# Performance work log

Hardware: AMD Instinct MI355X
Metric: run time of the kernel (lower is better)

The kernel has to match this reference:

```python
import jax, jax.numpy as jnp
import numpy as np


def _gcn_conv(h_in, W, b, src, dst, dinv):
    # GCNConv with symmetric normalization and self-loops:
    # out_i = sum_{j->i} dinv_j*dinv_i * (x_j W) + dinv_i^2 * (x_i W) + b
    n = h_in.shape[0]
    h = h_in @ W  # [N, C_out] -- transform before aggregation (PyG order)
    coef = dinv[src] * dinv[dst]  # [E]
    agg = jax.ops.segment_sum(h[src] * coef[:, None], dst, num_segments=n)
    return agg + h * (dinv * dinv)[:, None] + b


def setup_inputs() -> dict:
    key = jax.random.key(0)
    ks = jax.random.split(key, 9)
    N, E = 100000, 1600000
    C_in, C_h, C_out = 256, 128, 64
    x = jax.random.normal(ks[0], (N, C_in), dtype=jnp.float32)
    edge_index = jax.random.randint(ks[1], (2, E), 0, N, dtype=jnp.int64)
    eps = jax.random.normal(ks[2], (N, C_out), dtype=jnp.float32)
    s = 1.0 / np.sqrt(C_in)
    W1 = jax.random.uniform(ks[3], (C_in, C_h), jnp.float32, -s, s)
    b1 = jnp.zeros((C_h,), jnp.float32)
    sh = 1.0 / np.sqrt(C_h)
    Wmu = jax.random.uniform(ks[4], (C_h, C_out), jnp.float32, -sh, sh)
    bmu = jnp.zeros((C_out,), jnp.float32)
    Wlv = jax.random.uniform(ks[5], (C_h, C_out), jnp.float32, -sh, sh)
    blv = jnp.zeros((C_out,), jnp.float32)
    return {"x": x, "edge_index": edge_index, "eps": eps,
            "W1": W1, "b1": b1, "Wmu": Wmu, "bmu": bmu,
            "Wlv": Wlv, "blv": blv}


def reference(x, edge_index, eps, W1, b1, Wmu, bmu, Wlv, blv):
    n = x.shape[0]
    src, dst = edge_index[0], edge_index[1]
    # degree with self-loops (each node gets +1)
    deg = jax.ops.segment_sum(jnp.ones_like(dst, dtype=x.dtype), dst,
                              num_segments=n) + 1.0
    dinv = jax.lax.rsqrt(deg)
    # encoder (eval mode: dropout is identity)
    h = jax.nn.relu(_gcn_conv(x, W1, b1, src, dst, dinv))
    mu = _gcn_conv(h, Wmu, bmu, src, dst, dinv)
    logvar = _gcn_conv(h, Wlv, blv, src, dst, dinv)
    # reparameterization with provided noise: z = mu + eps * exp(0.5*logvar)
    z = mu + eps * jnp.exp(0.5 * logvar)
    # inner-product decoder on the given edges: sigmoid(<z_i, z_j>)
    dec = jax.nn.sigmoid(jnp.sum(z[src] * z[dst], axis=1))
    return z, mu, logvar, dec
```

## Files before the change

### kernel.cpp

```cpp
#include <hip/hip_runtime.h>
#include <hip/hip_bf16.h>

#define MAXD 64
#define NPB 128
#define BSHIFT 7
#define EB 8192
#define NBMAX 1024

typedef __attribute__((ext_vector_type(8))) short bf16x8;
typedef __attribute__((ext_vector_type(4))) float f32x4;

__device__ __forceinline__ float blo(unsigned u){ return __uint_as_float(u << 16); }
__device__ __forceinline__ float bhi(unsigned u){ return __uint_as_float(u & 0xffff0000u); }
__device__ __forceinline__ short cvbf(float f){ return (short)__bfloat16_as_ushort(__float2bfloat16(f)); }
__device__ __forceinline__ unsigned pk2(float a, float b){
  unsigned la = (unsigned)__bfloat16_as_ushort(__float2bfloat16(a));
  unsigned lb = (unsigned)__bfloat16_as_ushort(__float2bfloat16(b));
  return la | (lb << 16);
}

__global__ __launch_bounds__(256) void k_tr_all(const float* __restrict__ W1,
                                                const float* __restrict__ Wmu,
                                                const float* __restrict__ Wlv,
                                                __hip_bfloat16* __restrict__ W1T,
                                                __hip_bfloat16* __restrict__ WcT){
  int i = blockIdx.x * 256 + threadIdx.x;
  if (i < 32768){
    int k = i >> 7, c = i & 127;
    W1T[(size_t)c * 256 + k] = __float2bfloat16(W1[i]);
  } else if (i < 40960){
    int j = i - 32768;
    int k = j >> 6, c = j & 63;
    WcT[(size_t)c * 128 + k] = __float2bfloat16(Wmu[j]);
  } else if (i < 49152){
    int j = i - 40960;
    int k = j >> 6, c = j & 63;
    WcT[(size_t)(64 + c) * 128 + k] = __float2bfloat16(Wlv[j]);
  }
}

#define LDP 40
template<bool AF32>
__device__ __forceinline__ void gemm_body(short* As, short* Bs, const void* __restrict__ Av,
                                          const __hip_bfloat16* __restrict__ BT,
                                          __hip_bfloat16* __restrict__ C,
                                          int M, int K, int bid){
  int t = threadIdx.x;
  int wave = t >> 6, lane = t & 63;
  int rowbase = bid * 64;

  f32x4 zero4 = {0.f, 0.f, 0.f, 0.f};
  f32x4 acc[8];
  #pragma unroll
  for (int f = 0; f < 8; ++f) acc[f] = zero4;

  for (int k0 = 0; k0 < K; k0 += 32){
    {
      int r = t >> 2, p = t & 3;
      int grow = rowbase + r;
      bf16x8 v = {0,0,0,0,0,0,0,0};
      if (grow < M){
        if (AF32){
          const float* ap = (const float*)Av + (size_t)grow * K + k0 + p * 8;
          float4 f0 = *(const float4*)ap;
          float4 f1 = *(const float4*)(ap + 4);
          v[0] = cvbf(f0.x); v[1] = cvbf(f0.y); v[2] = cvbf(f0.z); v[3] = cvbf(f0.w);
          v[4] = cvbf(f1.x); v[5] = cvbf(f1.y); v[6] = cvbf(f1.z); v[7] = cvbf(f1.w);
        } else {
          const __hip_bfloat16* ap = (const __hip_bfloat16*)Av + (size_t)grow * K + k0 + p * 8;
          v = *(const bf16x8*)ap;
        }
      }
      *(bf16x8*)&As[r * LDP + p * 8] = v;
    }
    #pragma unroll
    for (int q = 0; q < 2; ++q){
      int idx = t + q * 256;
      int c = idx >> 2, p = idx & 3;
      bf16x8 v = *(const bf16x8*)&BT[(size_t)c * K + k0 + p * 8];
      *(bf16x8*)&Bs[c * LDP + p * 8] = v;
    }
    __syncthreads();
    int ks = (lane >> 4) * 8;
    bf16x8 afrag = *(const bf16x8*)&As[(wave * 16 + (lane & 15)) * LDP + ks];
    #pragma unroll
    for (int f = 0; f < 8; ++f){
      bf16x8 bfrag = *(const bf16x8*)&Bs[(f * 16 + (lane & 15)) * LDP + ks];
      acc[f] = __builtin_amdgcn_mfma_f32_16x16x32_bf16(afrag, bfrag, acc[f], 0, 0, 0);
    }
    __syncthreads();
  }
  int col0 = lane & 15;
  int r0 = wave * 16 + (lane >> 4) * 4;
  #pragma unroll
  for (int f = 0; f < 8; ++f){
    #pragma unroll
    for (int r = 0; r < 4; ++r){
      int grow = rowbase + r0 + r;
      if (grow < M) C[(size_t)grow * 128 + f * 16 + col0] = __float2bfloat16(acc[f][r]);
    }
  }
}

__global__ __launch_bounds__(256) void k_fused1(const float* __restrict__ x,
                                                const __hip_bfloat16* __restrict__ W1T,
                                                __hip_bfloat16* __restrict__ hlin, int M,
                                                const int* __restrict__ dst,
                                                int* __restrict__ blockHist,
                                                int E, int Gg, int HB, int NB){
  __shared__ short As[64 * LDP];
  __shared__ short Bs[128 * LDP];
  __shared__ int hsh[NBMAX];
  int t = threadIdx.x;
  if ((int)blockIdx.x < Gg){
    gemm_body<true>(As, Bs, x, W1T, hlin, M, 256, blockIdx.x);
  } else {
    int blk = blockIdx.x - Gg;
    for (int i = t; i < NB; i += 256) hsh[i] = 0;
    __syncthreads();
    int lo = blk * EB, hi = min(lo + EB, E);
    for (int j = lo + t; j < hi; j += 256){
      atomicAdd(&hsh[dst[j] >> BSHIFT], 1);
    }
    __syncthreads();
    for (int i = t; i < NB; i += 256) blockHist[(size_t)i * HB + blk] = hsh[i];
  }
}

__global__ __launch_bounds__(256) void k_scan_a(int* __restrict__ bh,
                                                int* __restrict__ rowTotal, int HB){
  int b = blockIdx.x, t = threadIdx.x;
  __shared__ int s[256];
  __shared__ int carry_s;
  if (t == 0) carry_s = 0;
  __syncthreads();
  for (int c0 = 0; c0 < HB; c0 += 256){
    int i = c0 + t;
    int v = (i < HB) ? bh[(size_t)b * HB + i] : 0;
    s[t] = v; __syncthreads();
    for (int off = 1; off < 256; off <<= 1){
      int x = (t >= off) ? s[t - off] : 0;
      __syncthreads();
      s[t] += x;
      __syncthreads();
    }
    int excl = (t == 0 ? 0 : s[t - 1]) + carry_s;
    if (i < HB) bh[(size_t)b * HB + i] = excl;
    __syncthreads();
    if (t == 255) carry_s = excl + v;
    __syncthreads();
  }
  if (t == 0) rowTotal[b] = carry_s;
}

__global__ __launch_bounds__(256) void k_scan_b(const int* __restrict__ rowTotal,
                                                int* __restrict__ rowOffset, int NB){
  int t = threadIdx.x;
  __shared__ int s[256];
  __shared__ int carry_s;
  if (t == 0) carry_s = 0;
  __syncthreads();
  for (int c0 = 0; c0 < NB; c0 += 256){
    int i = c0 + t;
    int v = (i < NB) ? rowTotal[i] : 0;
    s[t] = v; __syncthreads();
    for (int off = 1; off < 256; off <<= 1){
      int x = (t >= off) ? s[t - off] : 0;
      __syncthreads();
      s[t] += x;
      __syncthreads();
    }
    int excl = (t == 0 ? 0 : s[t - 1]) + carry_s;
    if (i < NB) rowOffset[i] = excl;
    __syncthreads();
    if (t == 255) carry_s = excl + v;
    __syncthreads();
  }
  if (t == 0) rowOffset[NB] = carry_s;
}

__global__ __launch_bounds__(256) void k_scatter(const int* __restrict__ src,
                                                 const int* __restrict__ dst,
                                                 const int* __restrict__ bh,
                                                 const int* __restrict__ rowOffset,
                                                 int2* __restrict__ P,
                                                 int E, int HB, int NB){
  int blk = blockIdx.x, t = threadIdx.x;
  __shared__ int cur[NBMAX];
  for (int i = t; i < NB; i += 256)
    cur[i] = rowOffset[i] + bh[(size_t)i * HB + blk];
  __syncthreads();
  int lo = blk * EB, hi = min(lo + EB, E);
  for (int j = lo + t; j < hi; j += 256){
    int s = src[j], d = dst[j];
    int pos = atomicAdd(&cur[d >> BSHIFT], 1);
    P[pos] = make_int2(s, d);
  }
}

__global__ __launch_bounds__(256) void k_build(const int2* __restrict__ P,
                                               const int* __restrict__ rowOffset,
                                               int* __restrict__ slots,
                                               int* __restrict__ cnt, int n){
  int b = blockIdx.x, t = threadIdx.x;
  int base = b * NPB;
  __shared__ int lcnt[NPB];
  __shared__ int lell[NPB * MAXD];
  if (t < NPB) lcnt[t] = 0;
  __syncthreads();
  int lo = rowOffset[b], hi = rowOffset[b + 1];
  for (int j = lo + t; j < hi; j += 256){
    int2 e = P[j];
    int loc = e.y - base;
    int pos = atomicAdd(&lcnt[loc], 1);
    if (pos < MAXD) lell[loc * MAXD + pos] = e.x;
  }
  __syncthreads();
  if (t < NPB && base + t < n){
    int m = lcnt[t];
    cnt[base + t] = m;
    int mm = m > MAXD ? MAXD : m;
    int* dstp = slots + (size_t)(base + t) * MAXD;
    for (int p = 0; p * 4 < mm; ++p)
      *(int4*)(dstp + p * 4) = *(int4*)(lell + t * MAXD + p * 4);
  }
}

#define LDH 136
__global__ __launch_bounds__(512, 8) void k_aggmm(const __hip_bfloat16* __restrict__ hlin,
                                                  const int* __restrict__ slots,
                                                  const int* __restrict__ cnt,
                                                  const float* __restrict__ b1,
                                                  const __hip_bfloat16* __restrict__ BT,
                                                  __hip_bfloat16* __restrict__ C, int n){
  __shared__ short Hs[64 * LDH];
  __shared__ short Bs[128 * LDP];
  int t = threadIdx.x;
  int wave = t >> 6, lane = t & 63;
  int g = lane >> 4, c = lane & 15;
  int nodebase = blockIdx.x * 64;

  for (int i = 0; i < 8; ++i){
    int node = nodebase + (wave << 3) + i;
    float a[8] = {0.f,0.f,0.f,0.f,0.f,0.f,0.f,0.f};
    auto acc8 = [&](uint4 v, float f){
      a[0]=fmaf(f,blo(v.x),a[0]); a[1]=fmaf(f,bhi(v.x),a[1]);
      a[2]=fmaf(f,blo(v.y),a[2]); a[3]=fmaf(f,bhi(v.y),a[3]);
      a[4]=fmaf(f,blo(v.z),a[4]); a[5]=fmaf(f,bhi(v.z),a[5]);
      a[6]=fmaf(f,blo(v.w),a[6]); a[7]=fmaf(f,bhi(v.w),a[7]);
    };
    if (node < n){
      int degt = cnt[node];
      float di = rsqrtf((float)degt + 1.0f);
      int deg = degt > MAXD ? MAXD : degt;
      int s_k = node; float c_k = 0.f;
      if (lane < deg){
        s_k = slots[(size_t)node * MAXD + lane];
        c_k = di * rsqrtf((float)cnt[s_k] + 1.0f);
      }
      for (int k0 = 0; k0 < deg; k0 += 16){
        int s0=__shfl(s_k,k0+g), s1=__shfl(s_k,k0+4+g), s2=__shfl(s_k,k0+8+g), s3=__shfl(s_k,k0+12+g);
        float f0=__shfl(c_k,k0+g), f1=__shfl(c_k,k0+4+g), f2=__shfl(c_k,k0+8+g), f3=__shfl(c_k,k0+12+g);
        uint4 v0 = *(const uint4*)(hlin + (size_t)s0*128 + c*8);
        uint4 v1 = *(const uint4*)(hlin + (size_t)s1*128 + c*8);
        uint4 v2 = *(const uint4*)(hlin + (size_t)s2*128 + c*8);
        uint4 v3 = *(const uint4*)(hlin + (size_t)s3*128 + c*8);
        acc8(v0,f0); acc8(v1,f1); acc8(v2,f2); acc8(v3,f3);
      }
      #pragma unroll
      for (int j = 0; j < 8; ++j){
        a[j] += __shfl_xor(a[j], 16);
        a[j] += __shfl_xor(a[j], 32);
      }
      uint4 sv = *(const uint4*)(hlin + (size_t)node*128 + c*8);
      acc8(sv, di * di);
      float4 bA = *(const float4*)(b1 + c*8);
      float4 bB = *(const float4*)(b1 + c*8 + 4);
      a[0]+=bA.x; a[1]+=bA.y; a[2]+=bA.z; a[3]+=bA.w;
      a[4]+=bB.x; a[5]+=bB.y; a[6]+=bB.z; a[7]+=bB.w;
      #pragma unroll
      for (int j = 0; j < 8; ++j) a[j] = fmaxf(a[j], 0.f);
    }
    if (g == 0){
      uint4 o;
      o.x = pk2(a[0],a[1]); o.y = pk2(a[2],a[3]);
      o.z = pk2(a[4],a[5]); o.w = pk2(a[6],a[7]);
      *(uint4*)&Hs[((wave << 3) + i) * LDH + c*8] = o;
    }
  }

  int wr = wave & 3, wc = wave >> 2;
  f32x4 zero4 = {0.f, 0.f, 0.f, 0.f};
  f32x4 acc[4];
  #pragma unroll
  for (int f = 0; f < 4; ++f) acc[f] = zero4;

  for (int k0 = 0; k0 < 128; k0 += 32){
    __syncthreads();
    {
      int cc = t >> 2, p = t & 3;
      bf16x8 v = *(const bf16x8*)&BT[(size_t)cc * 128 + k0 + p * 8];
      *(bf16x8*)&Bs[cc * LDP + p * 8] = v;
    }
    __syncthreads();
    int ks = (lane >> 4) * 8;
    bf16x8 afrag = *(const bf16x8*)&Hs[(wr * 16 + (lane & 15)) * LDH + k0 + ks];
    #pragma unroll
    for (int f = 0; f < 4; ++f){
      bf16x8 bfrag = *(const bf16x8*)&Bs[(wc * 64 + f * 16 + (lane & 15)) * LDP + ks];
      acc[f] = __builtin_amdgcn_mfma_f32_16x16x32_bf16(afrag, bfrag, acc[f], 0, 0, 0);
    }
  }
  int col0 = wc * 64 + (lane & 15);
  int r0 = wr * 16 + (lane >> 4) * 4;
  #pragma unroll
  for (int f = 0; f < 4; ++f){
    #pragma unroll
    for (int r = 0; r < 4; ++r){
      int grow = nodebase + r0 + r;
      if (grow < n) C[(size_t)grow * 128 + f * 16 + col0] = __float2bfloat16(acc[f][r]);
    }
  }
}

__global__ __launch_bounds__(256) void k_agg2(const __hip_bfloat16* __restrict__ hml,
                                              const int* __restrict__ slots,
                                              const int* __restrict__ cnt,
                                              const float* __restrict__ bmu,
                                              const float* __restrict__ blv,
                                              const float* __restrict__ eps,
                                              float* __restrict__ outz,
                                              float* __restrict__ outmu,
                                              float* __restrict__ outlv,
                                              __hip_bfloat16* __restrict__ z16, int n){
  int node = blockIdx.x * 4 + (threadIdx.x >> 6);
  if (node >= n) return;
  int lane = threadIdx.x & 63;
  int g = lane >> 4, c = lane & 15;
  int degt = cnt[node];
  float di = rsqrtf((float)degt + 1.0f);
  int deg = degt > MAXD ? MAXD : degt;

  int s_k = node; float c_k = 0.f;
  if (lane < deg){
    s_k = slots[(size_t)node * MAXD + lane];
    c_k = di * rsqrtf((float)cnt[s_k] + 1.0f);
  }

  float a[8] = {0.f,0.f,0.f,0.f,0.f,0.f,0.f,0.f};
  auto acc8 = [&](uint4 v, float f){
    a[0]=fmaf(f,blo(v.x),a[0]); a[1]=fmaf(f,bhi(v.x),a[1]);
    a[2]=fmaf(f,blo(v.y),a[2]); a[3]=fmaf(f,bhi(v.y),a[3]);
    a[4]=fmaf(f,blo(v.z),a[4]); a[5]=fmaf(f,bhi(v.z),a[5]);
    a[6]=fmaf(f,blo(v.w),a[6]); a[7]=fmaf(f,bhi(v.w),a[7]);
  };

  for (int k0 = 0; k0 < deg; k0 += 16){
    int s0=__shfl(s_k,k0+g), s1=__shfl(s_k,k0+4+g), s2=__shfl(s_k,k0+8+g), s3=__shfl(s_k,k0+12+g);
    float f0=__shfl(c_k,k0+g), f1=__shfl(c_k,k0+4+g), f2=__shfl(c_k,k0+8+g), f3=__shfl(c_k,k0+12+g);
    uint4 v0 = *(const uint4*)(hml + (size_t)s0*128 + c*8);
    uint4 v1 = *(const uint4*)(hml + (size_t)s1*128 + c*8);
    uint4 v2 = *(const uint4*)(hml + (size_t)s2*128 + c*8);
    uint4 v3 = *(const uint4*)(hml + (size_t)s3*128 + c*8);
    acc8(v0,f0); acc8(v1,f1); acc8(v2,f2); acc8(v3,f3);
  }
  #pragma unroll
  for (int j = 0; j < 8; ++j){
    a[j] += __shfl_xor(a[j], 16);
    a[j] += __shfl_xor(a[j], 32);
  }
  uint4 sv = *(const uint4*)(hml + (size_t)node*128 + c*8);
  acc8(sv, di * di);
  const float* bp = (c < 8) ? (bmu + c*8) : (blv + (c-8)*8);
  float4 bA = *(const float4*)bp;
  float4 bB = *(const float4*)(bp + 4);
  a[0]+=bA.x; a[1]+=bA.y; a[2]+=bA.z; a[3]+=bA.w;
  a[4]+=bB.x; a[5]+=bB.y; a[6]+=bB.z; a[7]+=bB.w;
  float p[8];
  #pragma unroll
  for (int j = 0; j < 8; ++j) p[j] = __shfl_xor(a[j], 8);
  if (g == 0){
    if (c < 8){
      float4 eA = *(const float4*)(eps + (size_t)node*64 + c*8);
      float4 eB = *(const float4*)(eps + (size_t)node*64 + c*8 + 4);
      float z[8];
      z[0]=fmaf(eA.x, __expf(0.5f*p[0]), a[0]); z[1]=fmaf(eA.y, __expf(0.5f*p[1]), a[1]);
      z[2]=fmaf(eA.z, __expf(0.5f*p[2]), a[2]); z[3]=fmaf(eA.w, __expf(0.5f*p[3]), a[3]);
      z[4]=fmaf(eB.x, __expf(0.5f*p[4]), a[4]); z[5]=fmaf(eB.y, __expf(0.5f*p[5]), a[5]);
      z[6]=fmaf(eB.z, __expf(0.5f*p[6]), a[6]); z[7]=fmaf(eB.w, __expf(0.5f*p[7]), a[7]);
      *(float4*)(outz + (size_t)node*64 + c*8)     = make_float4(z[0],z[1],z[2],z[3]);
      *(float4*)(outz + (size_t)node*64 + c*8 + 4) = make_float4(z[4],z[5],z[6],z[7]);
      *(float4*)(outmu + (size_t)node*64 + c*8)     = make_float4(a[0],a[1],a[2],a[3]);
      *(float4*)(outmu + (size_t)node*64 + c*8 + 4) = make_float4(a[4],a[5],a[6],a[7]);
      uint4 o;
      o.x = pk2(z[0],z[1]); o.y = pk2(z[2],z[3]);
      o.z = pk2(z[4],z[5]); o.w = pk2(z[6],z[7]);
      *(uint4*)(z16 + (size_t)node*64 + c*8) = o;
    } else {
      int cc = c - 8;
      *(float4*)(outlv + (size_t)node*64 + cc*8)     = make_float4(a[0],a[1],a[2],a[3]);
      *(float4*)(outlv + (size_t)node*64 + cc*8 + 4) = make_float4(a[4],a[5],a[6],a[7]);
    }
  }
}

__global__ __launch_bounds__(256) void k_dec(const int* __restrict__ src,
                                             const int* __restrict__ dst,
                                             const __hip_bfloat16* __restrict__ z16,
                                             float* __restrict__ dec, int E){
  int t = blockIdx.x * 256 + threadIdx.x;
  int e0 = (t >> 4) * 4;
  if (e0 >= E) return;
  int sl = t & 15;
  int eA = e0, eB = min(e0+1, E-1), eC = min(e0+2, E-1), eD = min(e0+3, E-1);
  int sA = src[eA], dA = dst[eA];
  int sB = src[eB], dB = dst[eB];
  int sC = src[eC], dC = dst[eC];
  int sD = src[eD], dD = dst[eD];
  uint2 a0 = *(const uint2*)(z16 + (size_t)sA*64 + sl*4);
  uint2 b0 = *(const uint2*)(z16 + (size_t)dA*64 + sl*4);
  uint2 a1 = *(const uint2*)(z16 + (size_t)sB*64 + sl*4);
  uint2 b1 = *(const uint2*)(z16 + (size_t)dB*64 + sl*4);
  uint2 a2 = *(const uint2*)(z16 + (size_t)sC*64 + sl*4);
  uint2 b2 = *(const uint2*)(z16 + (size_t)dC*64 + sl*4);
  uint2 a3 = *(const uint2*)(z16 + (size_t)sD*64 + sl*4);
  uint2 b3 = *(const uint2*)(z16 + (size_t)dD*64 + sl*4);
  float t0 = blo(a0.x)*blo(b0.x) + bhi(a0.x)*bhi(b0.x) + blo(a0.y)*blo(b0.y) + bhi(a0.y)*bhi(b0.y);
  float t1 = blo(a1.x)*blo(b1.x) + bhi(a1.x)*bhi(b1.x) + blo(a1.y)*blo(b1.y) + bhi(a1.y)*bhi(b1.y);
  float t2 = blo(a2.x)*blo(b2.x) + bhi(a2.x)*bhi(b2.x) + blo(a2.y)*blo(b2.y) + bhi(a2.y)*bhi(b2.y);
  float t3 = blo(a3.x)*blo(b3.x) + bhi(a3.x)*bhi(b3.x) + blo(a3.y)*blo(b3.y) + bhi(a3.y)*bhi(b3.y);
  #pragma unroll
  for (int m = 1; m <= 8; m <<= 1){
    t0 += __shfl_xor(t0, m);
    t1 += __shfl_xor(t1, m);
    t2 += __shfl_xor(t2, m);
    t3 += __shfl_xor(t3, m);
  }
  if (sl == 0){
    if (e0 + 3 < E){
      *(float4*)(dec + e0) = make_float4(1.f/(1.f+__expf(-t0)), 1.f/(1.f+__expf(-t1)),
                                         1.f/(1.f+__expf(-t2)), 1.f/(1.f+__expf(-t3)));
    } else {
      float r[4] = {1.f/(1.f+__expf(-t0)), 1.f/(1.f+__expf(-t1)),
                    1.f/(1.f+__expf(-t2)), 1.f/(1.f+__expf(-t3))};
      for (int j = 0; j < 4 && e0 + j < E; ++j) dec[e0 + j] = r[j];
    }
  }
}

extern "C" void kernel_launch(void* const* d_in, const int* in_sizes, int n_in,
                              void* d_out, int out_size, void* d_ws, size_t ws_size,
                              hipStream_t stream){
  const float* x   = (const float*)d_in[0];
  const int*   ei  = (const int*)d_in[1];
  const float* eps = (const float*)d_in[2];
  const float* W1  = (const float*)d_in[3];
  const float* b1  = (const float*)d_in[4];
  const float* Wmu = (const float*)d_in[5];
  const float* bmu = (const float*)d_in[6];
  const float* Wlv = (const float*)d_in[7];
  const float* blv = (const float*)d_in[8];

  int N = in_sizes[0] / 256;
  int E = in_sizes[1] / 2;
  const int* src = ei;
  const int* dst = ei + E;

  int NB = (N + NPB - 1) / NPB;
  int HB = (E + EB - 1) / EB;

  char* w = (char*)d_ws;
  auto alloc = [&](size_t bytes) -> char* {
    char* p = w; w += (bytes + 255) & ~(size_t)255; return p;
  };
  int*            cnt       = (int*) alloc((size_t)N * 4);
  int*            blockHist = (int*) alloc((size_t)NB * HB * 4);
  int*            rowTotal  = (int*) alloc((size_t)NB * 4);
  int*            rowOffset = (int*) alloc((size_t)(NB + 1) * 4);
  int*            slots     = (int*) alloc((size_t)N * MAXD * 4);
  __hip_bfloat16* hlin      = (__hip_bfloat16*) alloc((size_t)N * 128 * 2);
  __hip_bfloat16* hmulv     = (__hip_bfloat16*) alloc((size_t)N * 128 * 2);
  __hip_bfloat16* W1T       = (__hip_bfloat16*) alloc((size_t)256 * 128 * 2);
  __hip_bfloat16* WcT       = (__hip_bfloat16*) alloc((size_t)128 * 128 * 2);
  int2*           P         = (int2*) alloc((size_t)E * 8);

  __hip_bfloat16* z16 = (__hip_bfloat16*)P;

  float* oz   = (float*)d_out;
  float* omu  = oz  + (size_t)N * 64;
  float* olv  = omu + (size_t)N * 64;
  float* odec = olv + (size_t)N * 64;

  k_tr_all<<<(49152 + 255) / 256, 256, 0, stream>>>(W1, Wmu, Wlv, W1T, WcT);

  int Gg = (N + 63) / 64;
  k_fused1<<<Gg + HB, 256, 0, stream>>>(x, W1T, hlin, N, dst, blockHist, E, Gg, HB, NB);

  k_scan_a<<<NB, 256, 0, stream>>>(blockHist, rowTotal, HB);
  k_scan_b<<<1, 256, 0, stream>>>(rowTotal, rowOffset, NB);
  k_scatter<<<HB, 256, 0, stream>>>(src, dst, blockHist, rowOffset, P, E, HB, NB);
  k_build<<<NB, 256, 0, stream>>>(P, rowOffset, slots, cnt, N);

  k_aggmm<<<(N + 63) / 64, 512, 0, stream>>>(hlin, slots, cnt, b1, WcT, hmulv, N);

  k_agg2<<<(N + 3) / 4, 256, 0, stream>>>(hmulv, slots, cnt, bmu, blv, eps,
                                          oz, omu, olv, z16, N);

  int quads = (E + 3) / 4;
  k_dec<<<((size_t)quads * 16 + 255) / 256, 256, 0, stream>>>(src, dst, z16, odec, E);
}
```

Before: 274.5 us.

## Aggregate one node per 16-lane group and precompute dinv in build

Each 16-lane quarter-wave now owns one destination node in the aggregation kernels, where before four groups split one node's neighbours and then reduced with cross-group shuffles. Neighbours are fetched 16 at a time with a fixed unrolled first chunk and a tail loop. The inverse-sqrt degrees are computed once in k_build and stored, which replaces per-neighbour rsqrt of cnt. This aims to cut reduction shuffles and idle lanes on low-degree nodes and to raise memory-level parallelism, at the cost of more divergence for high-degree nodes and a lower occupancy hint on k_aggmm.

```diff
diff --git a/kernel.cpp b/kernel.cpp
--- a/kernel.cpp
+++ b/kernel.cpp
@@ -201,7 +201,8 @@
 __global__ __launch_bounds__(256) void k_build(const int2* __restrict__ P,
                                                const int* __restrict__ rowOffset,
                                                int* __restrict__ slots,
-                                               int* __restrict__ cnt, int n){
+                                               int* __restrict__ cnt,
+                                               float* __restrict__ dinv, int n){
   int b = blockIdx.x, t = threadIdx.x;
   int base = b * NPB;
   __shared__ int lcnt[NPB];
@@ -219,6 +220,7 @@
   if (t < NPB && base + t < n){
     int m = lcnt[t];
     cnt[base + t] = m;
+    dinv[base + t] = rsqrtf((float)m + 1.0f);
     int mm = m > MAXD ? MAXD : m;
     int* dstp = slots + (size_t)(base + t) * MAXD;
     for (int p = 0; p * 4 < mm; ++p)
@@ -226,10 +228,65 @@
   }
 }
 
+__device__ __forceinline__ void agg_rows(const __hip_bfloat16* __restrict__ tbl,
+                                         int node, int deg, float di,
+                                         int lane, int c,
+                                         const int* __restrict__ slots,
+                                         const float* __restrict__ dinv,
+                                         float* a){
+  auto acc8 = [&](uint4 v, float f){
+    a[0]=fmaf(f,blo(v.x),a[0]); a[1]=fmaf(f,bhi(v.x),a[1]);
+    a[2]=fmaf(f,blo(v.y),a[2]); a[3]=fmaf(f,bhi(v.y),a[3]);
+    a[4]=fmaf(f,blo(v.z),a[4]); a[5]=fmaf(f,bhi(v.z),a[5]);
+    a[6]=fmaf(f,blo(v.w),a[6]); a[7]=fmaf(f,bhi(v.w),a[7]);
+  };
+  size_t nbase = (size_t)node * MAXD;
+  int gb = lane & 48;
+  int sk0 = node; float ck0 = 0.f;
+  if (c < deg){ sk0 = slots[nbase + c]; ck0 = di * dinv[sk0]; }
+  #pragma unroll
+  for (int k0 = 0; k0 < 16; k0 += 4){
+    int   s0 = __shfl(sk0, gb + k0),     s1 = __shfl(sk0, gb + k0 + 1);
+    int   s2 = __shfl(sk0, gb + k0 + 2), s3 = __shfl(sk0, gb + k0 + 3);
+    float f0 = __shfl(ck0, gb + k0),     f1 = __shfl(ck0, gb + k0 + 1);
+    float f2 = __shfl(ck0, gb + k0 + 2), f3 = __shfl(ck0, gb + k0 + 3);
+    uint4 v0 = *(const uint4*)(tbl + (size_t)s0 * 128 + c * 8);
+    uint4 v1 = *(const uint4*)(tbl + (size_t)s1 * 128 + c * 8);
+    uint4 v2 = *(const uint4*)(tbl + (size_t)s2 * 128 + c * 8);
+    uint4 v3 = *(const uint4*)(tbl + (size_t)s3 * 128 + c * 8);
+    acc8(v0, f0); acc8(v1, f1); acc8(v2, f2); acc8(v3, f3);
+  }
+  if (deg > 16){
+    int sk1 = node; float ck1 = 0.f;
+    if (16 + c < deg){ sk1 = slots[nbase + 16 + c]; ck1 = di * dinv[sk1]; }
+    int d2 = (deg < 32 ? deg : 32) - 16;
+    for (int k0 = 0; k0 < d2; k0 += 4){
+      int   s0 = __shfl(sk1, gb + k0),     s1 = __shfl(sk1, gb + k0 + 1);
+      int   s2 = __shfl(sk1, gb + k0 + 2), s3 = __shfl(sk1, gb + k0 + 3);
+      float f0 = __shfl(ck1, gb + k0),     f1 = __shfl(ck1, gb + k0 + 1);
+      float f2 = __shfl(ck1, gb + k0 + 2), f3 = __shfl(ck1, gb + k0 + 3);
+      uint4 v0 = *(const uint4*)(tbl + (size_t)s0 * 128 + c * 8);
+      uint4 v1 = *(const uint4*)(tbl + (size_t)s1 * 128 + c * 8);
+      uint4 v2 = *(const uint4*)(tbl + (size_t)s2 * 128 + c * 8);
+      uint4 v3 = *(const uint4*)(tbl + (size_t)s3 * 128 + c * 8);
+      acc8(v0, f0); acc8(v1, f1); acc8(v2, f2); acc8(v3, f3);
+    }
+    for (int k = 32; k < deg; ++k){
+      int s = slots[nbase + k];
+      float f = di * dinv[s];
+      uint4 v = *(const uint4*)(tbl + (size_t)s * 128 + c * 8);
+      acc8(v, f);
+    }
+  }
+  uint4 sv = *(const uint4*)(tbl + (size_t)node * 128 + c * 8);
+  acc8(sv, di * di);
+}
+
 #define LDH 136
-__global__ __launch_bounds__(512, 8) void k_aggmm(const __hip_bfloat16* __restrict__ hlin,
+__global__ __launch_bounds__(512, 4) void k_aggmm(const __hip_bfloat16* __restrict__ hlin,
                                                   const int* __restrict__ slots,
                                                   const int* __restrict__ cnt,
+                                                  const float* __restrict__ dinv,
                                                   const float* __restrict__ b1,
                                                   const __hip_bfloat16* __restrict__ BT,
                                                   __hip_bfloat16* __restrict__ C, int n){
@@ -240,40 +297,16 @@
   int g = lane >> 4, c = lane & 15;
   int nodebase = blockIdx.x * 64;
 
-  for (int i = 0; i < 8; ++i){
-    int node = nodebase + (wave << 3) + i;
+  #pragma unroll
+  for (int pass = 0; pass < 2; ++pass){
+    int nl = pass * 32 + wave * 4 + g;
+    int node = nodebase + nl;
     float a[8] = {0.f,0.f,0.f,0.f,0.f,0.f,0.f,0.f};
-    auto acc8 = [&](uint4 v, float f){
-      a[0]=fmaf(f,blo(v.x),a[0]); a[1]=fmaf(f,bhi(v.x),a[1]);
-      a[2]=fmaf(f,blo(v.y),a[2]); a[3]=fmaf(f,bhi(v.y),a[3]);
-      a[4]=fmaf(f,blo(v.z),a[4]); a[5]=fmaf(f,bhi(v.z),a[5]);
-      a[6]=fmaf(f,blo(v.w),a[6]); a[7]=fmaf(f,bhi(v.w),a[7]);
-    };
     if (node < n){
       int degt = cnt[node];
-      float di = rsqrtf((float)degt + 1.0f);
+      float di = dinv[node];
       int deg = degt > MAXD ? MAXD : degt;
-      int s_k = node; float c_k = 0.f;
-      if (lane < deg){
-        s_k = slots[(size_t)node * MAXD + lane];
-        c_k = di * rsqrtf((float)cnt[s_k] + 1.0f);
-      }
-      for (int k0 = 0; k0 < deg; k0 += 16){
-        int s0=__shfl(s_k,k0+g), s1=__shfl(s_k,k0+4+g), s2=__shfl(s_k,k0+8+g), s3=__shfl(s_k,k0+12+g);
-        float f0=__shfl(c_k,k0+g), f1=__shfl(c_k,k0+4+g), f2=__shfl(c_k,k0+8+g), f3=__shfl(c_k,k0+12+g);
-        uint4 v0 = *(const uint4*)(hlin + (size_t)s0*128 + c*8);
-        uint4 v1 = *(const uint4*)(hlin + (size_t)s1*128 + c*8);
-        uint4 v2 = *(const uint4*)(hlin + (size_t)s2*128 + c*8);
-        uint4 v3 = *(const uint4*)(hlin + (size_t)s3*128 + c*8);
-        acc8(v0,f0); acc8(v1,f1); acc8(v2,f2); acc8(v3,f3);
-      }
-      #pragma unroll
-      for (int j = 0; j < 8; ++j){
-        a[j] += __shfl_xor(a[j], 16);
-        a[j] += __shfl_xor(a[j], 32);
-      }
-      uint4 sv = *(const uint4*)(hlin + (size_t)node*128 + c*8);
-      acc8(sv, di * di);
+      agg_rows(hlin, node, deg, di, lane, c, slots, dinv, a);
       float4 bA = *(const float4*)(b1 + c*8);
       float4 bB = *(const float4*)(b1 + c*8 + 4);
       a[0]+=bA.x; a[1]+=bA.y; a[2]+=bA.z; a[3]+=bA.w;
@@ -281,12 +314,10 @@
       #pragma unroll
       for (int j = 0; j < 8; ++j) a[j] = fmaxf(a[j], 0.f);
     }
-    if (g == 0){
-      uint4 o;
-      o.x = pk2(a[0],a[1]); o.y = pk2(a[2],a[3]);
-      o.z = pk2(a[4],a[5]); o.w = pk2(a[6],a[7]);
-      *(uint4*)&Hs[((wave << 3) + i) * LDH + c*8] = o;
-    }
+    uint4 o;
+    o.x = pk2(a[0],a[1]); o.y = pk2(a[2],a[3]);
+    o.z = pk2(a[4],a[5]); o.w = pk2(a[6],a[7]);
+    *(uint4*)&Hs[nl * LDH + c*8] = o;
   }
 
   int wr = wave & 3, wc = wave >> 2;
@@ -326,6 +357,7 @@
 __global__ __launch_bounds__(256) void k_agg2(const __hip_bfloat16* __restrict__ hml,
                                               const int* __restrict__ slots,
                                               const int* __restrict__ cnt,
+                                              const float* __restrict__ dinv,
                                               const float* __restrict__ bmu,
                                               const float* __restrict__ blv,
                                               const float* __restrict__ eps,
@@ -333,44 +365,17 @@
                                               float* __restrict__ outmu,
                                               float* __restrict__ outlv,
                                               __hip_bfloat16* __restrict__ z16, int n){
-  int node = blockIdx.x * 4 + (threadIdx.x >> 6);
-  if (node >= n) return;
   int lane = threadIdx.x & 63;
   int g = lane >> 4, c = lane & 15;
+  int node = blockIdx.x * 16 + (threadIdx.x >> 6) * 4 + g;
+  if (node >= n) return;
   int degt = cnt[node];
-  float di = rsqrtf((float)degt + 1.0f);
+  float di = dinv[node];
   int deg = degt > MAXD ? MAXD : degt;
 
-  int s_k = node; float c_k = 0.f;
-  if (lane < deg){
-    s_k = slots[(size_t)node * MAXD + lane];
-    c_k = di * rsqrtf((float)cnt[s_k] + 1.0f);
-  }
-
   float a[8] = {0.f,0.f,0.f,0.f,0.f,0.f,0.f,0.f};
-  auto acc8 = [&](uint4 v, float f){
-    a[0]=fmaf(f,blo(v.x),a[0]); a[1]=fmaf(f,bhi(v.x),a[1]);
-    a[2]=fmaf(f,blo(v.y),a[2]); a[3]=fmaf(f,bhi(v.y),a[3]);
-    a[4]=fmaf(f,blo(v.z),a[4]); a[5]=fmaf(f,bhi(v.z),a[5]);
-    a[6]=fmaf(f,blo(v.w),a[6]); a[7]=fmaf(f,bhi(v.w),a[7]);
-  };
-
-  for (int k0 = 0; k0 < deg; k0 += 16){
-    int s0=__shfl(s_k,k0+g), s1=__shfl(s_k,k0+4+g), s2=__shfl(s_k,k0+8+g), s3=__shfl(s_k,k0+12+g);
-    float f0=__shfl(c_k,k0+g), f1=__shfl(c_k,k0+4+g), f2=__shfl(c_k,k0+8+g), f3=__shfl(c_k,k0+12+g);
-    uint4 v0 = *(const uint4*)(hml + (size_t)s0*128 + c*8);
-    uint4 v1 = *(const uint4*)(hml + (size_t)s1*128 + c*8);
-    uint4 v2 = *(const uint4*)(hml + (size_t)s2*128 + c*8);
-    uint4 v3 = *(const uint4*)(hml + (size_t)s3*128 + c*8);
-    acc8(v0,f0); acc8(v1,f1); acc8(v2,f2); acc8(v3,f3);
-  }
-  #pragma unroll
-  for (int j = 0; j < 8; ++j){
-    a[j] += __shfl_xor(a[j], 16);
-    a[j] += __shfl_xor(a[j], 32);
-  }
-  uint4 sv = *(const uint4*)(hml + (size_t)node*128 + c*8);
-  acc8(sv, di * di);
+  agg_rows(hml, node, deg, di, lane, c, slots, dinv, a);
+
   const float* bp = (c < 8) ? (bmu + c*8) : (blv + (c-8)*8);
   float4 bA = *(const float4*)bp;
   float4 bB = *(const float4*)(bp + 4);
@@ -379,28 +384,26 @@
   float p[8];
   #pragma unroll
   for (int j = 0; j < 8; ++j) p[j] = __shfl_xor(a[j], 8);
-  if (g == 0){
-    if (c < 8){
-      float4 eA = *(const float4*)(eps + (size_t)node*64 + c*8);
-      float4 eB = *(const float4*)(eps + (size_t)node*64 + c*8 + 4);
-      float z[8];
-      z[0]=fmaf(eA.x, __expf(0.5f*p[0]), a[0]); z[1]=fmaf(eA.y, __expf(0.5f*p[1]), a[1]);
-      z[2]=fmaf(eA.z, __expf(0.5f*p[2]), a[2]); z[3]=fmaf(eA.w, __expf(0.5f*p[3]), a[3]);
-      z[4]=fmaf(eB.x, __expf(0.5f*p[4]), a[4]); z[5]=fmaf(eB.y, __expf(0.5f*p[5]), a[5]);
-      z[6]=fmaf(eB.z, __expf(0.5f*p[6]), a[6]); z[7]=fmaf(eB.w, __expf(0.5f*p[7]), a[7]);
-      *(float4*)(outz + (size_t)node*64 + c*8)     = make_float4(z[0],z[1],z[2],z[3]);
-      *(float4*)(outz + (size_t)node*64 + c*8 + 4) = make_float4(z[4],z[5],z[6],z[7]);
-      *(float4*)(outmu + (size_t)node*64 + c*8)     = make_float4(a[0],a[1],a[2],a[3]);
-      *(float4*)(outmu + (size_t)node*64 + c*8 + 4) = make_float4(a[4],a[5],a[6],a[7]);
-      uint4 o;
-      o.x = pk2(z[0],z[1]); o.y = pk2(z[2],z[3]);
-      o.z = pk2(z[4],z[5]); o.w = pk2(z[6],z[7]);
-      *(uint4*)(z16 + (size_t)node*64 + c*8) = o;
-    } else {
-      int cc = c - 8;
-      *(float4*)(outlv + (size_t)node*64 + cc*8)     = make_float4(a[0],a[1],a[2],a[3]);
-      *(float4*)(outlv + (size_t)node*64 + cc*8 + 4) = make_float4(a[4],a[5],a[6],a[7]);
-    }
+  if (c < 8){
+    float4 eA = *(const float4*)(eps + (size_t)node*64 + c*8);
+    float4 eB = *(const float4*)(eps + (size_t)node*64 + c*8 + 4);
+    float z[8];
+    z[0]=fmaf(eA.x, __expf(0.5f*p[0]), a[0]); z[1]=fmaf(eA.y, __expf(0.5f*p[1]), a[1]);
+    z[2]=fmaf(eA.z, __expf(0.5f*p[2]), a[2]); z[3]=fmaf(eA.w, __expf(0.5f*p[3]), a[3]);
+    z[4]=fmaf(eB.x, __expf(0.5f*p[4]), a[4]); z[5]=fmaf(eB.y, __expf(0.5f*p[5]), a[5]);
+    z[6]=fmaf(eB.z, __expf(0.5f*p[6]), a[6]); z[7]=fmaf(eB.w, __expf(0.5f*p[7]), a[7]);
+    *(float4*)(outz + (size_t)node*64 + c*8)     = make_float4(z[0],z[1],z[2],z[3]);
+    *(float4*)(outz + (size_t)node*64 + c*8 + 4) = make_float4(z[4],z[5],z[6],z[7]);
+    *(float4*)(outmu + (size_t)node*64 + c*8)     = make_float4(a[0],a[1],a[2],a[3]);
+    *(float4*)(outmu + (size_t)node*64 + c*8 + 4) = make_float4(a[4],a[5],a[6],a[7]);
+    uint4 o;
+    o.x = pk2(z[0],z[1]); o.y = pk2(z[2],z[3]);
+    o.z = pk2(z[4],z[5]); o.w = pk2(z[6],z[7]);
+    *(uint4*)(z16 + (size_t)node*64 + c*8) = o;
+  } else {
+    int cc = c - 8;
+    *(float4*)(outlv + (size_t)node*64 + cc*8)     = make_float4(a[0],a[1],a[2],a[3]);
+    *(float4*)(outlv + (size_t)node*64 + cc*8 + 4) = make_float4(a[4],a[5],a[6],a[7]);
   }
 }
 
@@ -474,6 +477,7 @@
     char* p = w; w += (bytes + 255) & ~(size_t)255; return p;
   };
   int*            cnt       = (int*) alloc((size_t)N * 4);
+  float*          dinv      = (float*) alloc((size_t)N * 4);
   int*            blockHist = (int*) alloc((size_t)NB * HB * 4);
   int*            rowTotal  = (int*) alloc((size_t)NB * 4);
   int*            rowOffset = (int*) alloc((size_t)(NB + 1) * 4);
@@ -499,12 +503,12 @@
   k_scan_a<<<NB, 256, 0, stream>>>(blockHist, rowTotal, HB);
   k_scan_b<<<1, 256, 0, stream>>>(rowTotal, rowOffset, NB);
   k_scatter<<<HB, 256, 0, stream>>>(src, dst, blockHist, rowOffset, P, E, HB, NB);
-  k_build<<<NB, 256, 0, stream>>>(P, rowOffset, slots, cnt, N);
-
-  k_aggmm<<<(N + 63) / 64, 512, 0, stream>>>(hlin, slots, cnt, b1, WcT, hmulv, N);
-
-  k_agg2<<<(N + 3) / 4, 256, 0, stream>>>(hmulv, slots, cnt, bmu, blv, eps,
-                                          oz, omu, olv, z16, N);
+  k_build<<<NB, 256, 0, stream>>>(P, rowOffset, slots, cnt, dinv, N);
+
+  k_aggmm<<<(N + 63) / 64, 512, 0, stream>>>(hlin, slots, cnt, dinv, b1, WcT, hmulv, N);
+
+  k_agg2<<<(N + 15) / 16, 256, 0, stream>>>(hmulv, slots, cnt, dinv, bmu, blv, eps,
+                                            oz, omu, olv, z16, N);
 
   int quads = (E + 3) / 4;
   k_dec<<<((size_t)quads * 16 + 255) / 256, 256, 0, stream>>>(src, dst, z16, odec, E);
```

Result: slower. 294.6 us (+7.3%).
